# Performance work log

Hardware: AMD Instinct MI355X
Metric: run time of the kernel (lower is better)

The kernel has to match this reference:

```python
import jax, jax.numpy as jnp
import numpy as np

N_NODES = 100000
N_EDGES = 1600000
IN_FEATS = 64
OUT_FEATS = 100


def setup_inputs() -> dict:
    key = jax.random.key(0)
    k1, k2, k3, k4 = jax.random.split(key, 4)
    e = jax.random.normal(k1, (N_EDGES, IN_FEATS), dtype=jnp.float32)
    dst = jax.random.randint(k2, (N_EDGES,), 0, N_NODES, dtype=jnp.int32)
    W = jax.random.normal(k3, (OUT_FEATS, IN_FEATS), dtype=jnp.float32) * (1.0 / np.sqrt(IN_FEATS))
    b = jax.random.normal(k4, (OUT_FEATS,), dtype=jnp.float32) * 0.01
    return {"e": e, "dst": dst, "W": W, "b": b, "n_nodes": N_NODES}


def reference(e, dst, W, b, n_nodes):
    # edge linear projection: f = e @ W^T + b  -> [n_edges, out_feats]
    f = jnp.einsum("ei,oi->eo", e, W) + b
    # copy_e + mean reduce: segment-mean of edge features into dst nodes
    sums = jax.ops.segment_sum(f, dst, num_segments=n_nodes)  # [n_nodes, out]
    deg = jax.ops.segment_sum(jnp.ones((f.shape[0],), dtype=f.dtype), dst,
                              num_segments=n_nodes)  # in-degree per node
    # DGL mean reducer yields 0 for zero-in-degree nodes
    h = sums / jnp.maximum(deg, 1.0)[:, None]
    return h
```

## Files before the change

kernel.cpp:

```cpp
#include <hip/hip_runtime.h>

#define N_NODES 100000
#define N_EDGES 1600000
#define IN_F    64
#define OUT_F   100

#define K_BUCKETS 1563
#define NBLK      500
#define EPB       3200
#define SCAN_LEN  (K_BUCKETS * NBLK)
#define SCH       2048
#define SB        ((SCAN_LEN + SCH - 1) / SCH)
#define CAP       3072

#define OFF_CNT   0
#define OFF_PART  (SCAN_LEN * 4)
#define OFF_BIN   (SCAN_LEN * 4 + 2048)
#define WS_NEEDED (OFF_BIN + N_EDGES * 4)

#define FB_DEG     0
#define FB_OFFS    524288
#define FB_CURSOR  1048576
#define FB_GCUR    1572864
#define FB_EIDS    1573888

__global__ void __launch_bounds__(256) k_count(const int* __restrict__ dst,
                                               int* __restrict__ cnt) {
    __shared__ int h[K_BUCKETS];
    for (int i = threadIdx.x; i < K_BUCKETS; i += 256) h[i] = 0;
    __syncthreads();
    int base = blockIdx.x * EPB;
    #pragma unroll
    for (int it = 0; it < 3; it++) {
        int i = base + it * 1024 + threadIdx.x * 4;
        int4 d = *(const int4*)(dst + i);
        atomicAdd(&h[d.x >> 6], 1);
        atomicAdd(&h[d.y >> 6], 1);
        atomicAdd(&h[d.z >> 6], 1);
        atomicAdd(&h[d.w >> 6], 1);
    }
    if (threadIdx.x < 128) {
        int i = base + 3072 + threadIdx.x;
        atomicAdd(&h[dst[i] >> 6], 1);
    }
    __syncthreads();
    for (int k = threadIdx.x; k < K_BUCKETS; k += 256)
        cnt[k * NBLK + blockIdx.x] = h[k];
}

__global__ void k_s1(const int* __restrict__ cnt, int* __restrict__ part) {
    __shared__ int ws_[4];
    int b0 = blockIdx.x * SCH;
    int t = threadIdx.x;
    int tot = 0;
    #pragma unroll
    for (int i = 0; i < 8; i++) {
        int idx = b0 + i * 256 + t;
        if (idx < SCAN_LEN) tot += cnt[idx];
    }
    #pragma unroll
    for (int off = 32; off; off >>= 1) tot += __shfl_down(tot, off, 64);
    if ((t & 63) == 0) ws_[t >> 6] = tot;
    __syncthreads();
    if (t == 0) part[blockIdx.x] = ws_[0] + ws_[1] + ws_[2] + ws_[3];
}

__global__ void k_s2(int* __restrict__ part) {
    int lane = threadIdx.x;
    int carry = 0;
    for (int b0 = 0; b0 < SB; b0 += 64) {
        int idx = b0 + lane;
        int v = (idx < SB) ? part[idx] : 0;
        int x = v;
        #pragma unroll
        for (int off = 1; off < 64; off <<= 1) {
            int y = __shfl_up(x, off, 64);
            if (lane >= off) x += y;
        }
        int tot = __shfl(x, 63, 64);
        if (idx < SB) part[idx] = carry + x - v;
        carry += tot;
    }
}

__global__ void k_s3(int* __restrict__ cnt, const int* __restrict__ part) {
    __shared__ int wsum[4];
    int t = threadIdx.x, lane = t & 63, w = t >> 6;
    int idx0 = blockIdx.x * SCH + t * 8;
    int v[8];
    int s = 0;
    #pragma unroll
    for (int i = 0; i < 8; i++) {
        v[i] = (idx0 + i < SCAN_LEN) ? cnt[idx0 + i] : 0;
        s += v[i];
    }
    int x = s;
    #pragma unroll
    for (int off = 1; off < 64; off <<= 1) {
        int y = __shfl_up(x, off, 64);
        if (lane >= off) x += y;
    }
    if (lane == 63) wsum[w] = x;
    __syncthreads();
    int wb = 0;
    for (int i = 0; i < w; i++) wb += wsum[i];
    int run = part[blockIdx.x] + wb + (x - s);
    #pragma unroll
    for (int i = 0; i < 8; i++) {
        int tmp = v[i];
        if (idx0 + i < SCAN_LEN) cnt[idx0 + i] = run;
        run += tmp;
    }
}

__global__ void __launch_bounds__(256) k_bin(const int* __restrict__ dst,
                                             const int* __restrict__ scn,
                                             int* __restrict__ binned) {
    __shared__ int cur[K_BUCKETS];
    for (int k = threadIdx.x; k < K_BUCKETS; k += 256)
        cur[k] = scn[k * NBLK + blockIdx.x];
    __syncthreads();
    int base = blockIdx.x * EPB;
    #pragma unroll
    for (int it = 0; it < 3; it++) {
        int i = base + it * 1024 + threadIdx.x * 4;
        int4 d = *(const int4*)(dst + i);
        int p;
        p = atomicAdd(&cur[d.x >> 6], 1); binned[p] = ((d.x & 63) << 21) | i;
        p = atomicAdd(&cur[d.y >> 6], 1); binned[p] = ((d.y & 63) << 21) | (i + 1);
        p = atomicAdd(&cur[d.z >> 6], 1); binned[p] = ((d.z & 63) << 21) | (i + 2);
        p = atomicAdd(&cur[d.w >> 6], 1); binned[p] = ((d.w & 63) << 21) | (i + 3);
    }
    if (threadIdx.x < 128) {
        int i = base + 3072 + threadIdx.x;
        int d = dst[i];
        int p = atomicAdd(&cur[d >> 6], 1);
        binned[p] = ((d & 63) << 21) | i;
    }
}

__global__ void __launch_bounds__(256, 2) k_fused(
        const float* __restrict__ e, const int* __restrict__ binned,
        const int* __restrict__ scn, const float* __restrict__ W,
        const float* __restrict__ b, float* __restrict__ out) {
    __shared__ int   deg[64];
    __shared__ int   lofs[64];
    __shared__ int   sorted[CAP];
    __shared__ __align__(16) float srow[4][64];

    int tid = threadIdx.x, lane = tid & 63, w = tid >> 6;
    int sub = lane & 15, g = lane >> 4;
    int bk = blockIdx.x;
    int base = scn[bk * NBLK];
    int end  = (bk + 1 < K_BUCKETS) ? scn[(bk + 1) * NBLK] : N_EDGES;
    int cntb = end - base;

    for (int i = tid; i < 64; i += 256) deg[i] = 0;
    __syncthreads();

    bool fast = (cntb <= CAP);
    if (fast) {
        int pk[12], rk[12];
        int nI = (cntb + 255) >> 8;
        for (int i = 0; i < nI; i++) {
            int idx = tid + i * 256;
            if (idx < cntb) {
                int p = binned[base + idx];
                pk[i] = p;
                rk[i] = atomicAdd(&deg[p >> 21], 1);
            } else pk[i] = -1;
        }
        __syncthreads();
        if (w == 0) {
            int d = deg[lane];
            int x = d;
            #pragma unroll
            for (int off = 1; off < 64; off <<= 1) {
                int y = __shfl_up(x, off, 64);
                if (lane >= off) x += y;
            }
            lofs[lane] = x - d;
        }
        __syncthreads();
        for (int i = 0; i < nI; i++) {
            if (pk[i] >= 0) {
                int lid = pk[i] >> 21;
                sorted[lofs[lid] + rk[i]] = pk[i] & 0x1FFFFF;
            }
        }
        __syncthreads();
    }

    int row1 = 64 + lane;
    if (row1 >= OUT_F) row1 = 0;
    float w0[IN_F], w1[IN_F];
    const float4* W4 = (const float4*)W;
    #pragma unroll
    for (int j = 0; j < IN_F / 4; j++) {
        float4 t0 = W4[lane * (IN_F / 4) + j];
        w0[4*j+0] = t0.x; w0[4*j+1] = t0.y; w0[4*j+2] = t0.z; w0[4*j+3] = t0.w;
        float4 t1 = W4[row1 * (IN_F / 4) + j];
        w1[4*j+0] = t1.x; w1[4*j+1] = t1.y; w1[4*j+2] = t1.z; w1[4*j+3] = t1.w;
    }
    float bb0 = b[lane];
    float bb1 = b[row1];

    const float4* e4 = (const float4*)e;

    for (int t = 0; t < 16; t++) {
        int lid = w * 16 + t;
        int node = bk * 64 + lid;
        if (node >= N_NODES) break;

        int c;
        float* sr = &srow[w][0];

        if (fast) {
            int o = lofs[lid];
            c = deg[lid];
            if (c > 0) {
                float4 a0 = {0,0,0,0}, a1 = {0,0,0,0}, a2 = {0,0,0,0}, a3 = {0,0,0,0};
                for (int cb = 0; cb < c; cb += 64) {
                    int cc = c - cb; if (cc > 64) cc = 64;
                    int ng = (cc + 3) >> 2;
                    int ob = o + cb;
                    for (int i = 0; i < ng; i += 4) {
                        int idx0 = (i + 0) * 4 + g;
                        int idx1 = (i + 1) * 4 + g;
                        int idx2 = (i + 2) * 4 + g;
                        int idx3 = (i + 3) * 4 + g;
                        int c1 = cc - 1;
                        int e0 = sorted[ob + ((idx0 < c1) ? idx0 : c1)];
                        int e1 = sorted[ob + ((idx1 < c1) ? idx1 : c1)];
                        int e2 = sorted[ob + ((idx2 < c1) ? idx2 : c1)];
                        int e3 = sorted[ob + ((idx3 < c1) ? idx3 : c1)];
                        float4 v0 = e4[(size_t)e0 * 16 + sub];
                        float4 v1 = e4[(size_t)e1 * 16 + sub];
                        float4 v2 = e4[(size_t)e2 * 16 + sub];
                        float4 v3 = e4[(size_t)e3 * 16 + sub];
                        float m0 = (idx0 < cc) ? 1.0f : 0.0f;
                        float m1 = (idx1 < cc) ? 1.0f : 0.0f;
                        float m2 = (idx2 < cc) ? 1.0f : 0.0f;
                        float m3 = (idx3 < cc) ? 1.0f : 0.0f;
                        a0.x = fmaf(v0.x, m0, a0.x); a0.y = fmaf(v0.y, m0, a0.y);
                        a0.z = fmaf(v0.z, m0, a0.z); a0.w = fmaf(v0.w, m0, a0.w);
                        a1.x = fmaf(v1.x, m1, a1.x); a1.y = fmaf(v1.y, m1, a1.y);
                        a1.z = fmaf(v1.z, m1, a1.z); a1.w = fmaf(v1.w, m1, a1.w);
                        a2.x = fmaf(v2.x, m2, a2.x); a2.y = fmaf(v2.y, m2, a2.y);
                        a2.z = fmaf(v2.z, m2, a2.z); a2.w = fmaf(v2.w, m2, a2.w);
                        a3.x = fmaf(v3.x, m3, a3.x); a3.y = fmaf(v3.y, m3, a3.y);
                        a3.z = fmaf(v3.z, m3, a3.z); a3.w = fmaf(v3.w, m3, a3.w);
                    }
                }
                float4 s;
                s.x = (a0.x + a1.x) + (a2.x + a3.x);
                s.y = (a0.y + a1.y) + (a2.y + a3.y);
                s.z = (a0.z + a1.z) + (a2.z + a3.z);
                s.w = (a0.w + a1.w) + (a2.w + a3.w);
                s.x += __shfl_xor(s.x, 16, 64);
                s.y += __shfl_xor(s.y, 16, 64);
                s.z += __shfl_xor(s.z, 16, 64);
                s.w += __shfl_xor(s.w, 16, 64);
                s.x += __shfl_xor(s.x, 32, 64);
                s.y += __shfl_xor(s.y, 32, 64);
                s.z += __shfl_xor(s.z, 32, 64);
                s.w += __shfl_xor(s.w, 32, 64);
                float inv = 1.0f / (float)c;
                s.x *= inv; s.y *= inv; s.z *= inv; s.w *= inv;
                if (g == 0) ((float4*)sr)[sub] = s;
            }
        } else {
            c = 0;
            float s0 = 0.f;
            for (int j0 = 0; j0 < cntb; j0 += 64) {
                int idx = j0 + lane;
                int p = (idx < cntb) ? binned[base + idx] : -1;
                bool m = (p >= 0) && ((p >> 21) == lid);
                unsigned long long msk = __ballot(m);
                c += __popcll(msk);
                while (msk) {
                    int l = __ffsll((long long)msk) - 1;
                    msk &= msk - 1;
                    int eid = __builtin_amdgcn_readlane(p, l) & 0x1FFFFF;
                    s0 += e[((size_t)eid << 6) + lane];
                }
            }
            if (c > 0) sr[lane] = s0 * (1.0f / (float)c);
        }

        float h0 = 0.0f, h1 = 0.0f;
        if (c > 0) {
            float aa0 = 0.f, aa1 = 0.f;
            const float4* sr4 = (const float4*)sr;
            #pragma unroll
            for (int q = 0; q < 16; q++) {
                float4 f = sr4[q];
                aa0 = fmaf(f.x, w0[4*q+0], aa0);  aa1 = fmaf(f.x, w1[4*q+0], aa1);
                aa0 = fmaf(f.y, w0[4*q+1], aa0);  aa1 = fmaf(f.y, w1[4*q+1], aa1);
                aa0 = fmaf(f.z, w0[4*q+2], aa0);  aa1 = fmaf(f.z, w1[4*q+2], aa1);
                aa0 = fmaf(f.w, w0[4*q+3], aa0);  aa1 = fmaf(f.w, w1[4*q+3], aa1);
            }
            h0 = aa0 + bb0;
            h1 = aa1 + bb1;
        }

        size_t ob2 = (size_t)node * OUT_F;
        out[ob2 + lane] = h0;
        if (lane < OUT_F - 64) out[ob2 + 64 + lane] = h1;
    }
}

__global__ void fb_hist(const int* __restrict__ dst, int* __restrict__ deg) {
    int i = (blockIdx.x * blockDim.x + threadIdx.x) * 4;
    if (i + 3 < N_EDGES) {
        int4 d = *(const int4*)(dst + i);
        atomicAdd(&deg[d.x], 1); atomicAdd(&deg[d.y], 1);
        atomicAdd(&deg[d.z], 1); atomicAdd(&deg[d.w], 1);
    } else {
        for (int k = i; k < N_EDGES; k++) atomicAdd(&deg[dst[k]], 1);
    }
}

__global__ void fb_scan(const int* __restrict__ deg, int* __restrict__ offs,
                        int* __restrict__ cursor, int* __restrict__ gcur) {
    int n = blockIdx.x * blockDim.x + threadIdx.x;
    int lane = threadIdx.x & 63;
    int d = (n < N_NODES) ? deg[n] : 0;
    int x = d;
    #pragma unroll
    for (int off = 1; off < 64; off <<= 1) {
        int y = __shfl_up(x, off, 64);
        if (lane >= off) x += y;
    }
    int excl = x - d;
    int total = __shfl(x, 63, 64);
    int bs = 0;
    if (lane == 63) bs = atomicAdd(gcur, total);
    bs = __shfl(bs, 63, 64);
    if (n < N_NODES) {
        offs[n] = bs + excl;
        cursor[n] = bs + excl;
    }
}

__global__ void fb_scatter(const int* __restrict__ dst, int* __restrict__ cursor,
                           int* __restrict__ eids) {
    int i = (blockIdx.x * blockDim.x + threadIdx.x) * 4;
    if (i + 3 < N_EDGES) {
        int4 d = *(const int4*)(dst + i);
        int p0 = atomicAdd(&cursor[d.x], 1);
        int p1 = atomicAdd(&cursor[d.y], 1);
        int p2 = atomicAdd(&cursor[d.z], 1);
        int p3 = atomicAdd(&cursor[d.w], 1);
        eids[p0] = i; eids[p1] = i + 1; eids[p2] = i + 2; eids[p3] = i + 3;
    } else {
        for (int k = i; k < N_EDGES; k++) {
            int pos = atomicAdd(&cursor[dst[k]], 1);
            eids[pos] = k;
        }
    }
}

__global__ void __launch_bounds__(256) fb_gather(
        const float* __restrict__ e, const int* __restrict__ eids,
        const int* __restrict__ offs, const int* __restrict__ deg,
        const float* __restrict__ W, const float* __restrict__ b,
        float* __restrict__ out, int n_waves_total) {
    __shared__ float srow[4][64];
    int lane = threadIdx.x & 63, w = (threadIdx.x >> 6) & 3;
    int wid  = (blockIdx.x * blockDim.x + threadIdx.x) >> 6;
    int row1 = 64 + lane;
    if (row1 >= OUT_F) row1 = 0;
    float w0[IN_F], w1[IN_F];
    const float4* W4 = (const float4*)W;
    #pragma unroll
    for (int j = 0; j < IN_F / 4; j++) {
        float4 t0 = W4[lane * (IN_F / 4) + j];
        w0[4*j+0] = t0.x; w0[4*j+1] = t0.y; w0[4*j+2] = t0.z; w0[4*j+3] = t0.w;
        float4 t1 = W4[row1 * (IN_F / 4) + j];
        w1[4*j+0] = t1.x; w1[4*j+1] = t1.y; w1[4*j+2] = t1.z; w1[4*j+3] = t1.w;
    }
    float bb0 = b[lane];
    float bb1 = b[row1];
    for (int n = wid; n < N_NODES; n += n_waves_total) {
        int o = __builtin_amdgcn_readfirstlane(offs[n]);
        int c = __builtin_amdgcn_readfirstlane(deg[n]);
        float s0 = 0.f, s1 = 0.f;
        for (int cb = 0; cb < c; cb += 64) {
            int cc = c - cb; if (cc > 64) cc = 64;
            int myeid = 0;
            if (lane < cc) myeid = eids[o + cb + lane];
            for (int j = 0; j < cc; j += 2) {
                int i0 = __builtin_amdgcn_readlane(myeid, j);
                s0 += e[((size_t)i0 << 6) + lane];
                if (j + 1 < cc) {
                    int i1 = __builtin_amdgcn_readlane(myeid, j + 1);
                    s1 += e[((size_t)i1 << 6) + lane];
                }
            }
        }
        float* sr = &srow[w][0];
        sr[lane] = (s0 + s1) * ((c > 0) ? 1.0f / (float)c : 0.0f);
        float a0 = 0.f, a1 = 0.f;
        const float4* sr4 = (const float4*)sr;
        #pragma unroll
        for (int q = 0; q < 16; q++) {
            float4 f = sr4[q];
            a0 = fmaf(f.x, w0[4*q+0], a0);  a1 = fmaf(f.x, w1[4*q+0], a1);
            a0 = fmaf(f.y, w0[4*q+1], a0);  a1 = fmaf(f.y, w1[4*q+1], a1);
            a0 = fmaf(f.z, w0[4*q+2], a0);  a1 = fmaf(f.z, w1[4*q+2], a1);
            a0 = fmaf(f.w, w0[4*q+3], a0);  a1 = fmaf(f.w, w1[4*q+3], a1);
        }
        float h0 = (c > 0) ? a0 + bb0 : 0.0f;
        float h1 = (c > 0) ? a1 + bb1 : 0.0f;
        size_t ob = (size_t)n * OUT_F;
        out[ob + lane] = h0;
        if (lane < OUT_F - 64) out[ob + 64 + lane] = h1;
    }
}

extern "C" void kernel_launch(void* const* d_in, const int* in_sizes, int n_in,
                              void* d_out, int out_size, void* d_ws, size_t ws_size,
                              hipStream_t stream) {
    const float* e   = (const float*)d_in[0];
    const int*   dst = (const int*)d_in[1];
    const float* W   = (const float*)d_in[2];
    const float* b   = (const float*)d_in[3];
    float* out = (float*)d_out;
    char* ws = (char*)d_ws;

    if (ws_size >= (size_t)WS_NEEDED) {
        int* cnt    = (int*)(ws + OFF_CNT);
        int* part   = (int*)(ws + OFF_PART);
        int* binned = (int*)(ws + OFF_BIN);

        k_count<<<NBLK, 256, 0, stream>>>(dst, cnt);
        k_s1   <<<SB, 256, 0, stream>>>(cnt, part);
        k_s2   <<<1, 64, 0, stream>>>(part);
        k_s3   <<<SB, 256, 0, stream>>>(cnt, part);
        k_bin  <<<NBLK, 256, 0, stream>>>(dst, cnt, binned);
        k_fused<<<K_BUCKETS, 256, 0, stream>>>(e, binned, cnt, W, b, out);
    } else {
        int* deg    = (int*)(ws + FB_DEG);
        int* offs   = (int*)(ws + FB_OFFS);
        int* cursor = (int*)(ws + FB_CURSOR);
        int* gcur   = (int*)(ws + FB_GCUR);
        int* eids   = (int*)(ws + FB_EIDS);

        hipMemsetAsync(deg, 0, N_NODES * sizeof(int), stream);
        hipMemsetAsync(gcur, 0, sizeof(int), stream);
        fb_hist   <<<(N_EDGES / 4 + 255) / 256, 256, 0, stream>>>(dst, deg);
        fb_scan   <<<(N_NODES + 255) / 256, 256, 0, stream>>>(deg, offs, cursor, gcur);
        fb_scatter<<<(N_EDGES / 4 + 255) / 256, 256, 0, stream>>>(dst, cursor, eids);
        fb_gather <<<8192, 256, 0, stream>>>(e, eids, offs, deg, W, b, out, 8192 * 4);
    }
}
```

Before: 648.2 us.

## Physically sort edge features by destination before per-node mean and projection

Adds a new primary path that builds a CSR over destination nodes with a histogram and scan, then scatters each full 64-float edge feature row into a dst-sorted buffer. A gather kernel then reads each node's edges contiguously, averages them and applies W and b once per node. The aim is to replace the bucketed random gathers of edge rows with streaming contiguous reads. The cost is an extra ~410MB write-plus-read of the feature matrix, a much larger workspace requirement, and atomic-ordered scatter writes. Edge order within a node now depends on the atomics, so float summation order is no longer deterministic.

```diff
diff --git a/kernel.cpp b/kernel.cpp
--- a/kernel.cpp
+++ b/kernel.cpp
@@ -4,6 +4,13 @@
 #define N_EDGES 1600000
 #define IN_F    64
 #define OUT_F   100
+
+#define NS_DEG    0
+#define NS_OFFS   (512 * 1024)
+#define NS_CUR    (1024 * 1024)
+#define NS_GCUR   (1536 * 1024)
+#define NS_ESORT  (2 * 1024 * 1024)
+#define NS_WS_NEEDED ((size_t)NS_ESORT + (size_t)N_EDGES * IN_F * 4)
 
 #define K_BUCKETS 1563
 #define NBLK      500
@@ -23,6 +30,164 @@
 #define FB_CURSOR  1048576
 #define FB_GCUR    1572864
 #define FB_EIDS    1573888
+
+
+__global__ void fb_hist(const int* __restrict__ dst, int* __restrict__ deg) {
+    int i = (blockIdx.x * blockDim.x + threadIdx.x) * 4;
+    if (i + 3 < N_EDGES) {
+        int4 d = *(const int4*)(dst + i);
+        atomicAdd(&deg[d.x], 1); atomicAdd(&deg[d.y], 1);
+        atomicAdd(&deg[d.z], 1); atomicAdd(&deg[d.w], 1);
+    } else {
+        for (int k = i; k < N_EDGES; k++) atomicAdd(&deg[dst[k]], 1);
+    }
+}
+
+__global__ void fb_scan(const int* __restrict__ deg, int* __restrict__ offs,
+                        int* __restrict__ cursor, int* __restrict__ gcur) {
+    int n = blockIdx.x * blockDim.x + threadIdx.x;
+    int lane = threadIdx.x & 63;
+    int d = (n < N_NODES) ? deg[n] : 0;
+    int x = d;
+    #pragma unroll
+    for (int off = 1; off < 64; off <<= 1) {
+        int y = __shfl_up(x, off, 64);
+        if (lane >= off) x += y;
+    }
+    int excl = x - d;
+    int total = __shfl(x, 63, 64);
+    int bs = 0;
+    if (lane == 63) bs = atomicAdd(gcur, total);
+    bs = __shfl(bs, 63, 64);
+    if (n < N_NODES) {
+        offs[n] = bs + excl;
+        cursor[n] = bs + excl;
+    }
+}
+
+__global__ void __launch_bounds__(256) ns_scatter(
+        const float* __restrict__ e, const int* __restrict__ dst,
+        int* __restrict__ cursor, float* __restrict__ es, int n_waves) {
+    int lane = threadIdx.x & 63;
+    int wid  = (blockIdx.x * blockDim.x + threadIdx.x) >> 6;
+    int sub = lane & 15, g = lane >> 4;
+    const float4* e4  = (const float4*)e;
+    float4*       es4 = (float4*)es;
+    const int EPI = 8;
+    const int TOT = N_EDGES / EPI;
+    for (int it = wid; it < TOT; it += n_waves) {
+        int base = it * EPI;
+        int p = 0;
+        if (lane < EPI) p = atomicAdd(&cursor[dst[base + lane]], 1);
+        #pragma unroll
+        for (int h = 0; h < 2; h++) {
+            int ph = __shfl(p, h * 4 + g, 64);
+            float4 v = e4[(size_t)(base + h * 4 + g) * 16 + sub];
+            es4[(size_t)ph * 16 + sub] = v;
+        }
+    }
+}
+
+__global__ void __launch_bounds__(256, 2) ns_gather(
+        const float* __restrict__ es, const int* __restrict__ offs,
+        const int* __restrict__ deg, const float* __restrict__ W,
+        const float* __restrict__ b, float* __restrict__ out, int n_waves) {
+    __shared__ __align__(16) float srow[4][64];
+    int lane = threadIdx.x & 63, w = threadIdx.x >> 6;
+    int sub = lane & 15, g = lane >> 4;
+    int wid  = (blockIdx.x * blockDim.x + threadIdx.x) >> 6;
+
+    int row1 = 64 + lane;
+    if (row1 >= OUT_F) row1 = 0;
+    float w0[IN_F], w1[IN_F];
+    const float4* W4 = (const float4*)W;
+    #pragma unroll
+    for (int j = 0; j < IN_F / 4; j++) {
+        float4 t0 = W4[lane * (IN_F / 4) + j];
+        w0[4*j+0] = t0.x; w0[4*j+1] = t0.y; w0[4*j+2] = t0.z; w0[4*j+3] = t0.w;
+        float4 t1 = W4[row1 * (IN_F / 4) + j];
+        w1[4*j+0] = t1.x; w1[4*j+1] = t1.y; w1[4*j+2] = t1.z; w1[4*j+3] = t1.w;
+    }
+    float bb0 = b[lane];
+    float bb1 = b[row1];
+
+    const float4* es4 = (const float4*)es;
+    float* sr = &srow[w][0];
+
+    for (int n = wid; n < N_NODES; n += n_waves) {
+        int o = __builtin_amdgcn_readfirstlane(offs[n]);
+        int c = __builtin_amdgcn_readfirstlane(deg[n]);
+        float h0 = 0.0f, h1 = 0.0f;
+        if (c > 0) {
+            float4 a0 = {0,0,0,0}, a1 = {0,0,0,0}, a2 = {0,0,0,0}, a3 = {0,0,0,0};
+            for (int cb = 0; cb < c; cb += 64) {
+                int cc = c - cb; if (cc > 64) cc = 64;
+                int ng = (cc + 3) >> 2;
+                int ob = o + cb;
+                for (int i = 0; i < ng; i += 4) {
+                    int idx0 = (i + 0) * 4 + g;
+                    int idx1 = (i + 1) * 4 + g;
+                    int idx2 = (i + 2) * 4 + g;
+                    int idx3 = (i + 3) * 4 + g;
+                    int c1 = cc - 1;
+                    int r0 = ob + ((idx0 < c1) ? idx0 : c1);
+                    int r1 = ob + ((idx1 < c1) ? idx1 : c1);
+                    int r2 = ob + ((idx2 < c1) ? idx2 : c1);
+                    int r3 = ob + ((idx3 < c1) ? idx3 : c1);
+                    float4 v0 = es4[(size_t)r0 * 16 + sub];
+                    float4 v1 = es4[(size_t)r1 * 16 + sub];
+                    float4 v2 = es4[(size_t)r2 * 16 + sub];
+                    float4 v3 = es4[(size_t)r3 * 16 + sub];
+                    float m0 = (idx0 < cc) ? 1.0f : 0.0f;
+                    float m1 = (idx1 < cc) ? 1.0f : 0.0f;
+                    float m2 = (idx2 < cc) ? 1.0f : 0.0f;
+                    float m3 = (idx3 < cc) ? 1.0f : 0.0f;
+                    a0.x = fmaf(v0.x, m0, a0.x); a0.y = fmaf(v0.y, m0, a0.y);
+                    a0.z = fmaf(v0.z, m0, a0.z); a0.w = fmaf(v0.w, m0, a0.w);
+                    a1.x = fmaf(v1.x, m1, a1.x); a1.y = fmaf(v1.y, m1, a1.y);
+                    a1.z = fmaf(v1.z, m1, a1.z); a1.w = fmaf(v1.w, m1, a1.w);
+                    a2.x = fmaf(v2.x, m2, a2.x); a2.y = fmaf(v2.y, m2, a2.y);
+                    a2.z = fmaf(v2.z, m2, a2.z); a2.w = fmaf(v2.w, m2, a2.w);
+                    a3.x = fmaf(v3.x, m3, a3.x); a3.y = fmaf(v3.y, m3, a3.y);
+                    a3.z = fmaf(v3.z, m3, a3.z); a3.w = fmaf(v3.w, m3, a3.w);
+                }
+            }
+            float4 s;
+            s.x = (a0.x + a1.x) + (a2.x + a3.x);
+            s.y = (a0.y + a1.y) + (a2.y + a3.y);
+            s.z = (a0.z + a1.z) + (a2.z + a3.z);
+            s.w = (a0.w + a1.w) + (a2.w + a3.w);
+            s.x += __shfl_xor(s.x, 16, 64);
+            s.y += __shfl_xor(s.y, 16, 64);
+            s.z += __shfl_xor(s.z, 16, 64);
+            s.w += __shfl_xor(s.w, 16, 64);
+            s.x += __shfl_xor(s.x, 32, 64);
+            s.y += __shfl_xor(s.y, 32, 64);
+            s.z += __shfl_xor(s.z, 32, 64);
+            s.w += __shfl_xor(s.w, 32, 64);
+            float inv = 1.0f / (float)c;
+            s.x *= inv; s.y *= inv; s.z *= inv; s.w *= inv;
+            if (g == 0) ((float4*)sr)[sub] = s;
+
+            float aa0 = 0.f, aa1 = 0.f;
+            const float4* sr4 = (const float4*)sr;
+            #pragma unroll
+            for (int q = 0; q < 16; q++) {
+                float4 f = sr4[q];
+                aa0 = fmaf(f.x, w0[4*q+0], aa0);  aa1 = fmaf(f.x, w1[4*q+0], aa1);
+                aa0 = fmaf(f.y, w0[4*q+1], aa0);  aa1 = fmaf(f.y, w1[4*q+1], aa1);
+                aa0 = fmaf(f.z, w0[4*q+2], aa0);  aa1 = fmaf(f.z, w1[4*q+2], aa1);
+                aa0 = fmaf(f.w, w0[4*q+3], aa0);  aa1 = fmaf(f.w, w1[4*q+3], aa1);
+            }
+            h0 = aa0 + bb0;
+            h1 = aa1 + bb1;
+        }
+        size_t ob2 = (size_t)n * OUT_F;
+        out[ob2 + lane] = h0;
+        if (lane < OUT_F - 64) out[ob2 + 64 + lane] = h1;
+    }
+}
+
 
 __global__ void __launch_bounds__(256) k_count(const int* __restrict__ dst,
                                                int* __restrict__ cnt) {
@@ -310,39 +475,6 @@
     }
 }
 
-__global__ void fb_hist(const int* __restrict__ dst, int* __restrict__ deg) {
-    int i = (blockIdx.x * blockDim.x + threadIdx.x) * 4;
-    if (i + 3 < N_EDGES) {
-        int4 d = *(const int4*)(dst + i);
-        atomicAdd(&deg[d.x], 1); atomicAdd(&deg[d.y], 1);
-        atomicAdd(&deg[d.z], 1); atomicAdd(&deg[d.w], 1);
-    } else {
-        for (int k = i; k < N_EDGES; k++) atomicAdd(&deg[dst[k]], 1);
-    }
-}
-
-__global__ void fb_scan(const int* __restrict__ deg, int* __restrict__ offs,
-                        int* __restrict__ cursor, int* __restrict__ gcur) {
-    int n = blockIdx.x * blockDim.x + threadIdx.x;
-    int lane = threadIdx.x & 63;
-    int d = (n < N_NODES) ? deg[n] : 0;
-    int x = d;
-    #pragma unroll
-    for (int off = 1; off < 64; off <<= 1) {
-        int y = __shfl_up(x, off, 64);
-        if (lane >= off) x += y;
-    }
-    int excl = x - d;
-    int total = __shfl(x, 63, 64);
-    int bs = 0;
-    if (lane == 63) bs = atomicAdd(gcur, total);
-    bs = __shfl(bs, 63, 64);
-    if (n < N_NODES) {
-        offs[n] = bs + excl;
-        cursor[n] = bs + excl;
-    }
-}
-
 __global__ void fb_scatter(const int* __restrict__ dst, int* __restrict__ cursor,
                            int* __restrict__ eids) {
     int i = (blockIdx.x * blockDim.x + threadIdx.x) * 4;
@@ -429,7 +561,20 @@
     float* out = (float*)d_out;
     char* ws = (char*)d_ws;
 
-    if (ws_size >= (size_t)WS_NEEDED) {
+    if (ws_size >= NS_WS_NEEDED) {
+        int*   deg    = (int*)(ws + NS_DEG);
+        int*   offs   = (int*)(ws + NS_OFFS);
+        int*   cursor = (int*)(ws + NS_CUR);
+        int*   gcur   = (int*)(ws + NS_GCUR);
+        float* es     = (float*)(ws + NS_ESORT);
+
+        hipMemsetAsync(deg, 0, N_NODES * sizeof(int), stream);
+        hipMemsetAsync(gcur, 0, sizeof(int), stream);
+        fb_hist   <<<(N_EDGES / 4 + 255) / 256, 256, 0, stream>>>(dst, deg);
+        fb_scan   <<<(N_NODES + 255) / 256, 256, 0, stream>>>(deg, offs, cursor, gcur);
+        ns_scatter<<<2048, 256, 0, stream>>>(e, dst, cursor, es, 2048 * 4);
+        ns_gather <<<2048, 256, 0, stream>>>(es, offs, deg, W, b, out, 2048 * 4);
+    } else if (ws_size >= (size_t)WS_NEEDED) {
         int* cnt    = (int*)(ws + OFF_CNT);
         int* part   = (int*)(ws + OFF_PART);
         int* binned = (int*)(ws + OFF_BIN);
```

New measurement: 841.6 us. 29.8% more time.

## Replace bucketed two-level binning with global atomic CSR build and prefetching gather

Applied to the files above, without the earlier changes.

Drops the per-block bucket histogram, three-stage scan, binning and in-block local sort. It builds a node-level CSR with global atomics (histogram, atomic-offset wave scan, scatter) instead. The gather kernel assigns 16 consecutive nodes per wave, keeps edge ids in registers and distributes them with shuffles rather than shared memory, and prefetches the next node's edge ids. This cuts kernel launches and shared-memory sorting, but relies on contended global atomics. Edge order within each node becomes nondeterministic, so the floating-point sum order can change between runs.

```diff
diff --git a/kernel.cpp b/kernel.cpp
--- a/kernel.cpp
+++ b/kernel.cpp
@@ -5,191 +5,78 @@
 #define IN_F    64
 #define OUT_F   100
 
-#define K_BUCKETS 1563
-#define NBLK      500
-#define EPB       3200
-#define SCAN_LEN  (K_BUCKETS * NBLK)
-#define SCH       2048
-#define SB        ((SCAN_LEN + SCH - 1) / SCH)
-#define CAP       3072
-
-#define OFF_CNT   0
-#define OFF_PART  (SCAN_LEN * 4)
-#define OFF_BIN   (SCAN_LEN * 4 + 2048)
-#define WS_NEEDED (OFF_BIN + N_EDGES * 4)
-
-#define FB_DEG     0
-#define FB_OFFS    524288
-#define FB_CURSOR  1048576
-#define FB_GCUR    1572864
-#define FB_EIDS    1573888
-
-__global__ void __launch_bounds__(256) k_count(const int* __restrict__ dst,
-                                               int* __restrict__ cnt) {
-    __shared__ int h[K_BUCKETS];
-    for (int i = threadIdx.x; i < K_BUCKETS; i += 256) h[i] = 0;
-    __syncthreads();
-    int base = blockIdx.x * EPB;
-    #pragma unroll
-    for (int it = 0; it < 3; it++) {
-        int i = base + it * 1024 + threadIdx.x * 4;
+#define WS_DEG     0
+#define WS_OFFS    (512 * 1024)
+#define WS_CUR     (1024 * 1024)
+#define WS_GCUR    (1536 * 1024)
+#define WS_EIDS    1573888
+#define WS_NEEDED  ((size_t)WS_EIDS + (size_t)N_EDGES * 4)
+
+__global__ void k_hist(const int* __restrict__ dst, int* __restrict__ deg) {
+    int i = (blockIdx.x * blockDim.x + threadIdx.x) * 4;
+    if (i + 3 < N_EDGES) {
         int4 d = *(const int4*)(dst + i);
-        atomicAdd(&h[d.x >> 6], 1);
-        atomicAdd(&h[d.y >> 6], 1);
-        atomicAdd(&h[d.z >> 6], 1);
-        atomicAdd(&h[d.w >> 6], 1);
-    }
-    if (threadIdx.x < 128) {
-        int i = base + 3072 + threadIdx.x;
-        atomicAdd(&h[dst[i] >> 6], 1);
-    }
-    __syncthreads();
-    for (int k = threadIdx.x; k < K_BUCKETS; k += 256)
-        cnt[k * NBLK + blockIdx.x] = h[k];
-}
-
-__global__ void k_s1(const int* __restrict__ cnt, int* __restrict__ part) {
-    __shared__ int ws_[4];
-    int b0 = blockIdx.x * SCH;
-    int t = threadIdx.x;
-    int tot = 0;
-    #pragma unroll
-    for (int i = 0; i < 8; i++) {
-        int idx = b0 + i * 256 + t;
-        if (idx < SCAN_LEN) tot += cnt[idx];
-    }
-    #pragma unroll
-    for (int off = 32; off; off >>= 1) tot += __shfl_down(tot, off, 64);
-    if ((t & 63) == 0) ws_[t >> 6] = tot;
-    __syncthreads();
-    if (t == 0) part[blockIdx.x] = ws_[0] + ws_[1] + ws_[2] + ws_[3];
-}
-
-__global__ void k_s2(int* __restrict__ part) {
-    int lane = threadIdx.x;
-    int carry = 0;
-    for (int b0 = 0; b0 < SB; b0 += 64) {
-        int idx = b0 + lane;
-        int v = (idx < SB) ? part[idx] : 0;
-        int x = v;
-        #pragma unroll
-        for (int off = 1; off < 64; off <<= 1) {
-            int y = __shfl_up(x, off, 64);
-            if (lane >= off) x += y;
-        }
-        int tot = __shfl(x, 63, 64);
-        if (idx < SB) part[idx] = carry + x - v;
-        carry += tot;
-    }
-}
-
-__global__ void k_s3(int* __restrict__ cnt, const int* __restrict__ part) {
-    __shared__ int wsum[4];
-    int t = threadIdx.x, lane = t & 63, w = t >> 6;
-    int idx0 = blockIdx.x * SCH + t * 8;
-    int v[8];
-    int s = 0;
-    #pragma unroll
-    for (int i = 0; i < 8; i++) {
-        v[i] = (idx0 + i < SCAN_LEN) ? cnt[idx0 + i] : 0;
-        s += v[i];
-    }
-    int x = s;
+        atomicAdd(&deg[d.x], 1); atomicAdd(&deg[d.y], 1);
+        atomicAdd(&deg[d.z], 1); atomicAdd(&deg[d.w], 1);
+    } else {
+        for (int k = i; k < N_EDGES; k++) atomicAdd(&deg[dst[k]], 1);
+    }
+}
+
+__global__ void k_scan(const int* __restrict__ deg, int* __restrict__ offs,
+                       int* __restrict__ cursor, int* __restrict__ gcur) {
+    int n = blockIdx.x * blockDim.x + threadIdx.x;
+    int lane = threadIdx.x & 63;
+    int d = (n < N_NODES) ? deg[n] : 0;
+    int x = d;
     #pragma unroll
     for (int off = 1; off < 64; off <<= 1) {
         int y = __shfl_up(x, off, 64);
         if (lane >= off) x += y;
     }
-    if (lane == 63) wsum[w] = x;
-    __syncthreads();
-    int wb = 0;
-    for (int i = 0; i < w; i++) wb += wsum[i];
-    int run = part[blockIdx.x] + wb + (x - s);
-    #pragma unroll
-    for (int i = 0; i < 8; i++) {
-        int tmp = v[i];
-        if (idx0 + i < SCAN_LEN) cnt[idx0 + i] = run;
-        run += tmp;
-    }
-}
-
-__global__ void __launch_bounds__(256) k_bin(const int* __restrict__ dst,
-                                             const int* __restrict__ scn,
-                                             int* __restrict__ binned) {
-    __shared__ int cur[K_BUCKETS];
-    for (int k = threadIdx.x; k < K_BUCKETS; k += 256)
-        cur[k] = scn[k * NBLK + blockIdx.x];
-    __syncthreads();
-    int base = blockIdx.x * EPB;
-    #pragma unroll
-    for (int it = 0; it < 3; it++) {
-        int i = base + it * 1024 + threadIdx.x * 4;
+    int excl = x - d;
+    int total = __shfl(x, 63, 64);
+    int bs = 0;
+    if (lane == 63) bs = atomicAdd(gcur, total);
+    bs = __shfl(bs, 63, 64);
+    if (n < N_NODES) {
+        offs[n] = bs + excl;
+        cursor[n] = bs + excl;
+    }
+}
+
+__global__ void k_scat(const int* __restrict__ dst, int* __restrict__ cursor,
+                       int* __restrict__ eids) {
+    int i = (blockIdx.x * blockDim.x + threadIdx.x) * 4;
+    if (i + 3 < N_EDGES) {
         int4 d = *(const int4*)(dst + i);
-        int p;
-        p = atomicAdd(&cur[d.x >> 6], 1); binned[p] = ((d.x & 63) << 21) | i;
-        p = atomicAdd(&cur[d.y >> 6], 1); binned[p] = ((d.y & 63) << 21) | (i + 1);
-        p = atomicAdd(&cur[d.z >> 6], 1); binned[p] = ((d.z & 63) << 21) | (i + 2);
-        p = atomicAdd(&cur[d.w >> 6], 1); binned[p] = ((d.w & 63) << 21) | (i + 3);
-    }
-    if (threadIdx.x < 128) {
-        int i = base + 3072 + threadIdx.x;
-        int d = dst[i];
-        int p = atomicAdd(&cur[d >> 6], 1);
-        binned[p] = ((d & 63) << 21) | i;
-    }
-}
-
-__global__ void __launch_bounds__(256, 2) k_fused(
-        const float* __restrict__ e, const int* __restrict__ binned,
-        const int* __restrict__ scn, const float* __restrict__ W,
-        const float* __restrict__ b, float* __restrict__ out) {
-    __shared__ int   deg[64];
-    __shared__ int   lofs[64];
-    __shared__ int   sorted[CAP];
+        int p0 = atomicAdd(&cursor[d.x], 1);
+        int p1 = atomicAdd(&cursor[d.y], 1);
+        int p2 = atomicAdd(&cursor[d.z], 1);
+        int p3 = atomicAdd(&cursor[d.w], 1);
+        eids[p0] = i; eids[p1] = i + 1; eids[p2] = i + 2; eids[p3] = i + 3;
+    } else {
+        for (int k = i; k < N_EDGES; k++) {
+            int pos = atomicAdd(&cursor[dst[k]], 1);
+            eids[pos] = k;
+        }
+    }
+}
+
+#define NPW 16
+__global__ void __launch_bounds__(256, 2) k_gather(
+        const float* __restrict__ e, const int* __restrict__ eids,
+        const int* __restrict__ offs, const int* __restrict__ deg,
+        const float* __restrict__ W, const float* __restrict__ b,
+        float* __restrict__ out) {
     __shared__ __align__(16) float srow[4][64];
-
-    int tid = threadIdx.x, lane = tid & 63, w = tid >> 6;
+    int lane = threadIdx.x & 63, w = threadIdx.x >> 6;
     int sub = lane & 15, g = lane >> 4;
-    int bk = blockIdx.x;
-    int base = scn[bk * NBLK];
-    int end  = (bk + 1 < K_BUCKETS) ? scn[(bk + 1) * NBLK] : N_EDGES;
-    int cntb = end - base;
-
-    for (int i = tid; i < 64; i += 256) deg[i] = 0;
-    __syncthreads();
-
-    bool fast = (cntb <= CAP);
-    if (fast) {
-        int pk[12], rk[12];
-        int nI = (cntb + 255) >> 8;
-        for (int i = 0; i < nI; i++) {
-            int idx = tid + i * 256;
-            if (idx < cntb) {
-                int p = binned[base + idx];
-                pk[i] = p;
-                rk[i] = atomicAdd(&deg[p >> 21], 1);
-            } else pk[i] = -1;
-        }
-        __syncthreads();
-        if (w == 0) {
-            int d = deg[lane];
-            int x = d;
-            #pragma unroll
-            for (int off = 1; off < 64; off <<= 1) {
-                int y = __shfl_up(x, off, 64);
-                if (lane >= off) x += y;
-            }
-            lofs[lane] = x - d;
-        }
-        __syncthreads();
-        for (int i = 0; i < nI; i++) {
-            if (pk[i] >= 0) {
-                int lid = pk[i] >> 21;
-                sorted[lofs[lid] + rk[i]] = pk[i] & 0x1FFFFF;
-            }
-        }
-        __syncthreads();
-    }
+    int wave = blockIdx.x * 4 + w;
+    int base = wave * NPW;
+    if (base >= N_NODES) return;
+    int nmax = N_NODES - base;
+    if (nmax > NPW) nmax = NPW;
 
     int row1 = 64 + lane;
     if (row1 >= OUT_F) row1 = 0;
@@ -205,91 +92,88 @@
     float bb0 = b[lane];
     float bb1 = b[row1];
 
+    int o_l = 0, d_l = 0;
+    if (lane < nmax) {
+        o_l = offs[base + lane];
+        d_l = deg[base + lane];
+    }
+
     const float4* e4 = (const float4*)e;
-
-    for (int t = 0; t < 16; t++) {
-        int lid = w * 16 + t;
-        int node = bk * 64 + lid;
-        if (node >= N_NODES) break;
-
-        int c;
-        float* sr = &srow[w][0];
-
-        if (fast) {
-            int o = lofs[lid];
-            c = deg[lid];
-            if (c > 0) {
-                float4 a0 = {0,0,0,0}, a1 = {0,0,0,0}, a2 = {0,0,0,0}, a3 = {0,0,0,0};
-                for (int cb = 0; cb < c; cb += 64) {
-                    int cc = c - cb; if (cc > 64) cc = 64;
-                    int ng = (cc + 3) >> 2;
-                    int ob = o + cb;
-                    for (int i = 0; i < ng; i += 4) {
-                        int idx0 = (i + 0) * 4 + g;
-                        int idx1 = (i + 1) * 4 + g;
-                        int idx2 = (i + 2) * 4 + g;
-                        int idx3 = (i + 3) * 4 + g;
-                        int c1 = cc - 1;
-                        int e0 = sorted[ob + ((idx0 < c1) ? idx0 : c1)];
-                        int e1 = sorted[ob + ((idx1 < c1) ? idx1 : c1)];
-                        int e2 = sorted[ob + ((idx2 < c1) ? idx2 : c1)];
-                        int e3 = sorted[ob + ((idx3 < c1) ? idx3 : c1)];
-                        float4 v0 = e4[(size_t)e0 * 16 + sub];
-                        float4 v1 = e4[(size_t)e1 * 16 + sub];
-                        float4 v2 = e4[(size_t)e2 * 16 + sub];
-                        float4 v3 = e4[(size_t)e3 * 16 + sub];
-                        float m0 = (idx0 < cc) ? 1.0f : 0.0f;
-                        float m1 = (idx1 < cc) ? 1.0f : 0.0f;
-                        float m2 = (idx2 < cc) ? 1.0f : 0.0f;
-                        float m3 = (idx3 < cc) ? 1.0f : 0.0f;
-                        a0.x = fmaf(v0.x, m0, a0.x); a0.y = fmaf(v0.y, m0, a0.y);
-                        a0.z = fmaf(v0.z, m0, a0.z); a0.w = fmaf(v0.w, m0, a0.w);
-                        a1.x = fmaf(v1.x, m1, a1.x); a1.y = fmaf(v1.y, m1, a1.y);
-                        a1.z = fmaf(v1.z, m1, a1.z); a1.w = fmaf(v1.w, m1, a1.w);
-                        a2.x = fmaf(v2.x, m2, a2.x); a2.y = fmaf(v2.y, m2, a2.y);
-                        a2.z = fmaf(v2.z, m2, a2.z); a2.w = fmaf(v2.w, m2, a2.w);
-                        a3.x = fmaf(v3.x, m3, a3.x); a3.y = fmaf(v3.y, m3, a3.y);
-                        a3.z = fmaf(v3.z, m3, a3.z); a3.w = fmaf(v3.w, m3, a3.w);
-                    }
-                }
-                float4 s;
-                s.x = (a0.x + a1.x) + (a2.x + a3.x);
-                s.y = (a0.y + a1.y) + (a2.y + a3.y);
-                s.z = (a0.z + a1.z) + (a2.z + a3.z);
-                s.w = (a0.w + a1.w) + (a2.w + a3.w);
-                s.x += __shfl_xor(s.x, 16, 64);
-                s.y += __shfl_xor(s.y, 16, 64);
-                s.z += __shfl_xor(s.z, 16, 64);
-                s.w += __shfl_xor(s.w, 16, 64);
-                s.x += __shfl_xor(s.x, 32, 64);
-                s.y += __shfl_xor(s.y, 32, 64);
-                s.z += __shfl_xor(s.z, 32, 64);
-                s.w += __shfl_xor(s.w, 32, 64);
-                float inv = 1.0f / (float)c;
-                s.x *= inv; s.y *= inv; s.z *= inv; s.w *= inv;
-                if (g == 0) ((float4*)sr)[sub] = s;
-            }
-        } else {
-            c = 0;
-            float s0 = 0.f;
-            for (int j0 = 0; j0 < cntb; j0 += 64) {
-                int idx = j0 + lane;
-                int p = (idx < cntb) ? binned[base + idx] : -1;
-                bool m = (p >= 0) && ((p >> 21) == lid);
-                unsigned long long msk = __ballot(m);
-                c += __popcll(msk);
-                while (msk) {
-                    int l = __ffsll((long long)msk) - 1;
-                    msk &= msk - 1;
-                    int eid = __builtin_amdgcn_readlane(p, l) & 0x1FFFFF;
-                    s0 += e[((size_t)eid << 6) + lane];
+    float* sr = &srow[w][0];
+
+    int id_next = 0;
+    {
+        int c0 = __shfl(d_l, 0, 64);
+        int o0 = __shfl(o_l, 0, 64);
+        int cc0 = (c0 < 64) ? c0 : 64;
+        if (lane < cc0) id_next = eids[o0 + lane];
+    }
+
+    for (int j = 0; j < nmax; j++) {
+        int id_cur = id_next;
+        int o = __shfl(o_l, j, 64);
+        int c = __shfl(d_l, j, 64);
+
+        if (j + 1 < nmax) {
+            int cn = __shfl(d_l, j + 1, 64);
+            int on = __shfl(o_l, j + 1, 64);
+            int ccn = (cn < 64) ? cn : 64;
+            if (lane < ccn) id_next = eids[on + lane];
+        }
+
+        float h0 = 0.0f, h1 = 0.0f;
+        if (c > 0) {
+            float4 a0 = {0,0,0,0}, a1 = {0,0,0,0}, a2 = {0,0,0,0}, a3 = {0,0,0,0};
+            for (int cb = 0; cb < c; cb += 64) {
+                int cc = c - cb; if (cc > 64) cc = 64;
+                int ids = id_cur;
+                if (cb > 0) ids = (lane < cc) ? eids[o + cb + lane] : 0;
+                int ng = (cc + 3) >> 2;
+                int c1 = cc - 1;
+                for (int i = 0; i < ng; i += 4) {
+                    int idx0 = (i + 0) * 4 + g;
+                    int idx1 = (i + 1) * 4 + g;
+                    int idx2 = (i + 2) * 4 + g;
+                    int idx3 = (i + 3) * 4 + g;
+                    int e0 = __shfl(ids, (idx0 < c1) ? idx0 : c1, 64);
+                    int e1 = __shfl(ids, (idx1 < c1) ? idx1 : c1, 64);
+                    int e2 = __shfl(ids, (idx2 < c1) ? idx2 : c1, 64);
+                    int e3 = __shfl(ids, (idx3 < c1) ? idx3 : c1, 64);
+                    float4 v0 = e4[(size_t)e0 * 16 + sub];
+                    float4 v1 = e4[(size_t)e1 * 16 + sub];
+                    float4 v2 = e4[(size_t)e2 * 16 + sub];
+                    float4 v3 = e4[(size_t)e3 * 16 + sub];
+                    float m0 = (idx0 < cc) ? 1.0f : 0.0f;
+                    float m1 = (idx1 < cc) ? 1.0f : 0.0f;
+                    float m2 = (idx2 < cc) ? 1.0f : 0.0f;
+                    float m3 = (idx3 < cc) ? 1.0f : 0.0f;
+                    a0.x = fmaf(v0.x, m0, a0.x); a0.y = fmaf(v0.y, m0, a0.y);
+                    a0.z = fmaf(v0.z, m0, a0.z); a0.w = fmaf(v0.w, m0, a0.w);
+                    a1.x = fmaf(v1.x, m1, a1.x); a1.y = fmaf(v1.y, m1, a1.y);
+                    a1.z = fmaf(v1.z, m1, a1.z); a1.w = fmaf(v1.w, m1, a1.w);
+                    a2.x = fmaf(v2.x, m2, a2.x); a2.y = fmaf(v2.y, m2, a2.y);
+                    a2.z = fmaf(v2.z, m2, a2.z); a2.w = fmaf(v2.w, m2, a2.w);
+                    a3.x = fmaf(v3.x, m3, a3.x); a3.y = fmaf(v3.y, m3, a3.y);
+                    a3.z = fmaf(v3.z, m3, a3.z); a3.w = fmaf(v3.w, m3, a3.w);
                 }
             }
-            if (c > 0) sr[lane] = s0 * (1.0f / (float)c);
-        }
-
-        float h0 = 0.0f, h1 = 0.0f;
-        if (c > 0) {
+            float4 s;
+            s.x = (a0.x + a1.x) + (a2.x + a3.x);
+            s.y = (a0.y + a1.y) + (a2.y + a3.y);
+            s.z = (a0.z + a1.z) + (a2.z + a3.z);
+            s.w = (a0.w + a1.w) + (a2.w + a3.w);
+            s.x += __shfl_xor(s.x, 16, 64);
+            s.y += __shfl_xor(s.y, 16, 64);
+            s.z += __shfl_xor(s.z, 16, 64);
+            s.w += __shfl_xor(s.w, 16, 64);
+            s.x += __shfl_xor(s.x, 32, 64);
+            s.y += __shfl_xor(s.y, 32, 64);
+            s.z += __shfl_xor(s.z, 32, 64);
+            s.w += __shfl_xor(s.w, 32, 64);
+            float inv = 1.0f / (float)c;
+            s.x *= inv; s.y *= inv; s.z *= inv; s.w *= inv;
+            if (g == 0) ((float4*)sr)[sub] = s;
+
             float aa0 = 0.f, aa1 = 0.f;
             const float4* sr4 = (const float4*)sr;
             #pragma unroll
@@ -304,118 +188,10 @@
             h1 = aa1 + bb1;
         }
 
+        int node = base + j;
         size_t ob2 = (size_t)node * OUT_F;
         out[ob2 + lane] = h0;
         if (lane < OUT_F - 64) out[ob2 + 64 + lane] = h1;
-    }
-}
-
-__global__ void fb_hist(const int* __restrict__ dst, int* __restrict__ deg) {
-    int i = (blockIdx.x * blockDim.x + threadIdx.x) * 4;
-    if (i + 3 < N_EDGES) {
-        int4 d = *(const int4*)(dst + i);
-        atomicAdd(&deg[d.x], 1); atomicAdd(&deg[d.y], 1);
-        atomicAdd(&deg[d.z], 1); atomicAdd(&deg[d.w], 1);
-    } else {
-        for (int k = i; k < N_EDGES; k++) atomicAdd(&deg[dst[k]], 1);
-    }
-}
-
-__global__ void fb_scan(const int* __restrict__ deg, int* __restrict__ offs,
-                        int* __restrict__ cursor, int* __restrict__ gcur) {
-    int n = blockIdx.x * blockDim.x + threadIdx.x;
-    int lane = threadIdx.x & 63;
-    int d = (n < N_NODES) ? deg[n] : 0;
-    int x = d;
-    #pragma unroll
-    for (int off = 1; off < 64; off <<= 1) {
-        int y = __shfl_up(x, off, 64);
-        if (lane >= off) x += y;
-    }
-    int excl = x - d;
-    int total = __shfl(x, 63, 64);
-    int bs = 0;
-    if (lane == 63) bs = atomicAdd(gcur, total);
-    bs = __shfl(bs, 63, 64);
-    if (n < N_NODES) {
-        offs[n] = bs + excl;
-        cursor[n] = bs + excl;
-    }
-}
-
-__global__ void fb_scatter(const int* __restrict__ dst, int* __restrict__ cursor,
-                           int* __restrict__ eids) {
-    int i = (blockIdx.x * blockDim.x + threadIdx.x) * 4;
-    if (i + 3 < N_EDGES) {
-        int4 d = *(const int4*)(dst + i);
-        int p0 = atomicAdd(&cursor[d.x], 1);
-        int p1 = atomicAdd(&cursor[d.y], 1);
-        int p2 = atomicAdd(&cursor[d.z], 1);
-        int p3 = atomicAdd(&cursor[d.w], 1);
-        eids[p0] = i; eids[p1] = i + 1; eids[p2] = i + 2; eids[p3] = i + 3;
-    } else {
-        for (int k = i; k < N_EDGES; k++) {
-            int pos = atomicAdd(&cursor[dst[k]], 1);
-            eids[pos] = k;
-        }
-    }
-}
-
-__global__ void __launch_bounds__(256) fb_gather(
-        const float* __restrict__ e, const int* __restrict__ eids,
-        const int* __restrict__ offs, const int* __restrict__ deg,
-        const float* __restrict__ W, const float* __restrict__ b,
-        float* __restrict__ out, int n_waves_total) {
-    __shared__ float srow[4][64];
-    int lane = threadIdx.x & 63, w = (threadIdx.x >> 6) & 3;
-    int wid  = (blockIdx.x * blockDim.x + threadIdx.x) >> 6;
-    int row1 = 64 + lane;
-    if (row1 >= OUT_F) row1 = 0;
-    float w0[IN_F], w1[IN_F];
-    const float4* W4 = (const float4*)W;
-    #pragma unroll
-    for (int j = 0; j < IN_F / 4; j++) {
-        float4 t0 = W4[lane * (IN_F / 4) + j];
-        w0[4*j+0] = t0.x; w0[4*j+1] = t0.y; w0[4*j+2] = t0.z; w0[4*j+3] = t0.w;
-        float4 t1 = W4[row1 * (IN_F / 4) + j];
-        w1[4*j+0] = t1.x; w1[4*j+1] = t1.y; w1[4*j+2] = t1.z; w1[4*j+3] = t1.w;
-    }
-    float bb0 = b[lane];
-    float bb1 = b[row1];
-    for (int n = wid; n < N_NODES; n += n_waves_total) {
-        int o = __builtin_amdgcn_readfirstlane(offs[n]);
-        int c = __builtin_amdgcn_readfirstlane(deg[n]);
-        float s0 = 0.f, s1 = 0.f;
-        for (int cb = 0; cb < c; cb += 64) {
-            int cc = c - cb; if (cc > 64) cc = 64;
-            int myeid = 0;
-            if (lane < cc) myeid = eids[o + cb + lane];
-            for (int j = 0; j < cc; j += 2) {
-                int i0 = __builtin_amdgcn_readlane(myeid, j);
-                s0 += e[((size_t)i0 << 6) + lane];
-                if (j + 1 < cc) {
-                    int i1 = __builtin_amdgcn_readlane(myeid, j + 1);
-                    s1 += e[((size_t)i1 << 6) + lane];
-                }
-            }
-        }
-        float* sr = &srow[w][0];
-        sr[lane] = (s0 + s1) * ((c > 0) ? 1.0f / (float)c : 0.0f);
-        float a0 = 0.f, a1 = 0.f;
-        const float4* sr4 = (const float4*)sr;
-        #pragma unroll
-        for (int q = 0; q < 16; q++) {
-            float4 f = sr4[q];
-            a0 = fmaf(f.x, w0[4*q+0], a0);  a1 = fmaf(f.x, w1[4*q+0], a1);
-            a0 = fmaf(f.y, w0[4*q+1], a0);  a1 = fmaf(f.y, w1[4*q+1], a1);
-            a0 = fmaf(f.z, w0[4*q+2], a0);  a1 = fmaf(f.z, w1[4*q+2], a1);
-            a0 = fmaf(f.w, w0[4*q+3], a0);  a1 = fmaf(f.w, w1[4*q+3], a1);
-        }
-        float h0 = (c > 0) ? a0 + bb0 : 0.0f;
-        float h1 = (c > 0) ? a1 + bb1 : 0.0f;
-        size_t ob = (size_t)n * OUT_F;
-        out[ob + lane] = h0;
-        if (lane < OUT_F - 64) out[ob + 64 + lane] = h1;
     }
 }
 
@@ -429,29 +205,20 @@
     float* out = (float*)d_out;
     char* ws = (char*)d_ws;
 
-    if (ws_size >= (size_t)WS_NEEDED) {
-        int* cnt    = (int*)(ws + OFF_CNT);
-        int* part   = (int*)(ws + OFF_PART);
-        int* binned = (int*)(ws + OFF_BIN);
-
-        k_count<<<NBLK, 256, 0, stream>>>(dst, cnt);
-        k_s1   <<<SB, 256, 0, stream>>>(cnt, part);
-        k_s2   <<<1, 64, 0, stream>>>(part);
-        k_s3   <<<SB, 256, 0, stream>>>(cnt, part);
-        k_bin  <<<NBLK, 256, 0, stream>>>(dst, cnt, binned);
-        k_fused<<<K_BUCKETS, 256, 0, stream>>>(e, binned, cnt, W, b, out);
-    } else {
-        int* deg    = (int*)(ws + FB_DEG);
-        int* offs   = (int*)(ws + FB_OFFS);
-        int* cursor = (int*)(ws + FB_CURSOR);
-        int* gcur   = (int*)(ws + FB_GCUR);
-        int* eids   = (int*)(ws + FB_EIDS);
-
-        hipMemsetAsync(deg, 0, N_NODES * sizeof(int), stream);
-        hipMemsetAsync(gcur, 0, sizeof(int), stream);
-        fb_hist   <<<(N_EDGES / 4 + 255) / 256, 256, 0, stream>>>(dst, deg);
-        fb_scan   <<<(N_NODES + 255) / 256, 256, 0, stream>>>(deg, offs, cursor, gcur);
-        fb_scatter<<<(N_EDGES / 4 + 255) / 256, 256, 0, stream>>>(dst, cursor, eids);
-        fb_gather <<<8192, 256, 0, stream>>>(e, eids, offs, deg, W, b, out, 8192 * 4);
-    }
-}
+    int* deg    = (int*)(ws + WS_DEG);
+    int* offs   = (int*)(ws + WS_OFFS);
+    int* cursor = (int*)(ws + WS_CUR);
+    int* gcur   = (int*)(ws + WS_GCUR);
+    int* eids   = (int*)(ws + WS_EIDS);
+
+    hipMemsetAsync(deg, 0, N_NODES * sizeof(int), stream);
+    hipMemsetAsync(gcur, 0, sizeof(int), stream);
+
+    k_hist<<<(N_EDGES / 4 + 255) / 256, 256, 0, stream>>>(dst, deg);
+    k_scan<<<(N_NODES + 255) / 256, 256, 0, stream>>>(deg, offs, cursor, gcur);
+    k_scat<<<(N_EDGES / 4 + 255) / 256, 256, 0, stream>>>(dst, cursor, eids);
+
+    int nwaves = (N_NODES + NPW - 1) / NPW;
+    int nblocks = (nwaves + 3) / 4;
+    k_gather<<<nblocks, 256, 0, stream>>>(e, eids, offs, deg, W, b, out);
+}
```

New measurement: 825.7 us. +27.4%, slower.
